# Optimization experiments

Measured on AMD Instinct MI355X. Metric: run time of the kernel, lower is better.

## Reference

```python
import jax, jax.numpy as jnp
import numpy as np

N_NODES = 100000
N_EDGES = 1600000
HIDDEN = 128
BN_EPS = 1e-5


def setup_inputs() -> dict:
    key = jax.random.key(0)
    ks = jax.random.split(key, 6)
    x0 = jax.random.normal(ks[0], (N_NODES, HIDDEN), dtype=jnp.float32)
    x1 = jax.random.normal(ks[1], (N_NODES, HIDDEN), dtype=jnp.float32)
    edge_index = jax.random.randint(ks[2], (2, N_EDGES), 0, N_NODES, dtype=jnp.int64)
    mean_weight = jnp.ones((2,), dtype=jnp.float32)
    # GIN MLP: Linear(h,h) -> ReLU -> Linear(h,h); scale ~ torch default init
    scale = 1.0 / np.sqrt(HIDDEN)
    W1 = jax.random.normal(ks[3], (HIDDEN, HIDDEN), dtype=jnp.float32) * scale
    b1 = jnp.zeros((HIDDEN,), dtype=jnp.float32)
    W2 = jax.random.normal(ks[4], (HIDDEN, HIDDEN), dtype=jnp.float32) * scale
    b2 = jnp.zeros((HIDDEN,), dtype=jnp.float32)
    gamma = jnp.ones((HIDDEN,), dtype=jnp.float32)
    beta = jnp.zeros((HIDDEN,), dtype=jnp.float32)
    return {"x0": x0, "x1": x1, "edge_index": edge_index,
            "mean_weight": mean_weight, "W1": W1, "b1": b1,
            "W2": W2, "b2": b2, "gamma": gamma, "beta": beta}


def reference(x0, x1, edge_index, mean_weight, W1, b1, W2, b2, gamma, beta):
    # sigmoid-gated sum of the two node-feature inputs (no drop-path: deterministic eval)
    s = jax.nn.sigmoid(mean_weight)
    out = s[0] * x0 + s[1] * x1                      # [N, H]
    # GINConv, eps=0: h = MLP(x + sum_{j in N(i)} x_j)
    src, dst = edge_index[0], edge_index[1]
    agg = jax.ops.segment_sum(out[src], dst, num_segments=out.shape[0])  # scatter-add [N, H]
    h = out + agg
    h = jnp.maximum(h @ W1 + b1, 0.0) @ W2 + b2      # Linear-ReLU-Linear
    # BatchNorm1d, training-mode batch statistics (biased variance)
    mean = jnp.mean(h, axis=0)
    var = jnp.var(h, axis=0)
    hn = (h - mean) * jax.lax.rsqrt(var + BN_EPS)
    return hn * gamma + beta
```

## Files before the change

### kernel.cpp

```cpp
#include <hip/hip_runtime.h>
#include <math.h>

#define N_NODES 100000
#define N_EDGES 1600000
#define HID 128
#define BN_EPS 1e-5f
#define BM 64
#define NTILES ((N_NODES + BM - 1) / BM)
#define MLP_BLOCKS 512
#define NSUB 16
#define NPW 4
#define BN_BLOCKS 512

typedef __attribute__((ext_vector_type(8))) short bf16x8;
typedef __attribute__((ext_vector_type(4))) float f32x4;

__device__ inline unsigned short f2bf(float f) {
    unsigned u = __float_as_uint(f);
    unsigned r = u + 0x7FFFu + ((u >> 16) & 1u);
    return (unsigned short)(r >> 16);
}
__device__ inline unsigned pk2(float lo, float hi) {
    return (unsigned)f2bf(lo) | ((unsigned)f2bf(hi) << 16);
}
__device__ inline float bflo(unsigned u) { return __uint_as_float(u << 16); }
__device__ inline float bfhi(unsigned u) { return __uint_as_float(u & 0xffff0000u); }

__global__ __launch_bounds__(256) void k_front(const float* __restrict__ x0,
                                               const float* __restrict__ x1,
                                               const float* __restrict__ mw,
                                               unsigned* __restrict__ gate_u2,
                                               float* __restrict__ shadow,
                                               const float* __restrict__ W1,
                                               const float* __restrict__ W2,
                                               unsigned short* __restrict__ W1T,
                                               unsigned short* __restrict__ W2T,
                                               const int* __restrict__ ei,
                                               int* __restrict__ head,
                                               int2* __restrict__ pair) {
    int bid = blockIdx.x, tid = threadIdx.x;
    int role = bid % 3;
    if (role < 2) {
        int gid = (bid / 3) * 2 + role;
        int t = gid * 256 + tid;
        if (gid < 64) {
            shadow[t] = 0.0f;
            int k = t >> 7, n = t & 127;
            W1T[n * HID + k] = f2bf(W1[t]);
            W2T[n * HID + k] = f2bf(W2[t]);
        }
        float s0 = 1.0f / (1.0f + expf(-mw[0]));
        float s1 = 1.0f / (1.0f + expf(-mw[1]));
        float4 a = ((const float4*)x0)[t];
        float4 b = ((const float4*)x1)[t];
        uint2 o;
        o.x = pk2(s0 * a.x + s1 * b.x, s0 * a.y + s1 * b.y);
        o.y = pk2(s0 * a.z + s1 * b.z, s0 * a.w + s1 * b.w);
        ((uint2*)gate_u2)[t] = o;
    } else {
        int e = (bid / 3) * 256 + tid;
        int src = ei[e];
        int dst = ei[N_EDGES + e];
        int old = atomicExch(&head[(e & (NSUB - 1)) * N_NODES + dst], e);
        pair[e] = make_int2(src, old);
    }
}

__global__ __launch_bounds__(256) void k_agg(const unsigned* __restrict__ gu,
                                             const int2* __restrict__ pair,
                                             const int* __restrict__ head,
                                             unsigned* __restrict__ hbuf_u) {
    int wid = threadIdx.x >> 6, lane = threadIdx.x & 63;
    int nbase = (blockIdx.x * 4 + wid) * NPW;
    int e = head[(lane & 15) * N_NODES + (nbase + (lane >> 4))];

    float sx[NPW], sy[NPW];
#pragma unroll
    for (int j = 0; j < NPW; ++j) {
        unsigned g = gu[(size_t)(nbase + j) * 64 + lane];
        sx[j] = bflo(g); sy[j] = bfhi(g);
    }

    while (__any(e >= 0)) {
        int2 pv = make_int2(-1, -1);
        if (e >= 0) pv = pair[e];
#pragma unroll
        for (int j = 0; j < 64; ++j) {
            int sv = __builtin_amdgcn_readlane(pv.x, j);
            if (sv >= 0) {
                unsigned v = gu[(size_t)sv * 64 + lane];
                sx[j >> 4] += bflo(v);
                sy[j >> 4] += bfhi(v);
            }
        }
        e = pv.y;
    }
#pragma unroll
    for (int j = 0; j < NPW; ++j)
        hbuf_u[(size_t)(nbase + j) * 64 + lane] = pk2(sx[j], sy[j]);
}

__global__ __launch_bounds__(256, 2) void k_mlp(unsigned short* __restrict__ hbuf,
                                                const unsigned short* __restrict__ W1T,
                                                const unsigned short* __restrict__ W2T,
                                                const float* __restrict__ b1,
                                                const float* __restrict__ b2,
                                                float* __restrict__ shadow) {
    __shared__ short lds_x[BM * HID];
    __shared__ short lds_w1[HID * HID];
    __shared__ short lds_w2[HID * HID];

    const int tid = threadIdx.x;

    for (int c = tid; c < 2048; c += 256) {
        int n = c >> 4, k16 = c & 15;
        int4 v1 = ((const int4*)W1T)[c];
        int4 v2 = ((const int4*)W2T)[c];
        int boff = n * 256 + ((k16 * 16) ^ ((n & 7) << 4));
        *(int4*)((char*)lds_w1 + boff) = v1;
        *(int4*)((char*)lds_w2 + boff) = v2;
    }

    const int wid = tid >> 6, lane = tid & 63;
    const int wrow = wid >> 1, wcol = wid & 1;
    const int l15 = lane & 15, l4 = lane >> 4;

    float b1g[4], b2g[4];
#pragma unroll
    for (int nf = 0; nf < 4; ++nf) {
        int n = wcol * 64 + nf * 16 + l15;
        b1g[nf] = b1[n];
        b2g[nf] = b2[n];
    }

    float psum[4] = {0.f, 0.f, 0.f, 0.f}, psq[4] = {0.f, 0.f, 0.f, 0.f};

    __syncthreads();

    for (int tile = blockIdx.x; tile < NTILES; tile += MLP_BLOCKS) {
        const int m0 = tile * BM;

        for (int c = tid; c < BM * 16; c += 256) {
            int r = c >> 4, k16 = c & 15;
            int row = m0 + r;
            int4 v = {0, 0, 0, 0};
            if (row < N_NODES)
                v = ((const int4*)(hbuf + (size_t)row * HID))[k16];
            int boff = r * 256 + ((k16 * 16) ^ ((r & 7) << 4));
            *(int4*)((char*)lds_x + boff) = v;
        }
        __syncthreads();

        f32x4 acc1[2][4];
#pragma unroll
        for (int mf = 0; mf < 2; ++mf)
#pragma unroll
            for (int nf = 0; nf < 4; ++nf) acc1[mf][nf] = (f32x4){0.f, 0.f, 0.f, 0.f};

#pragma unroll
        for (int kc = 0; kc < 4; ++kc) {
            bf16x8 av[2], bv[4];
#pragma unroll
            for (int mf = 0; mf < 2; ++mf) {
                int r = wrow * 32 + mf * 16 + l15;
                int boff = r * 256 + (((kc * 64) + l4 * 16) ^ ((r & 7) << 4));
                av[mf] = *(const bf16x8*)((const char*)lds_x + boff);
            }
#pragma unroll
            for (int nf = 0; nf < 4; ++nf) {
                int n = wcol * 64 + nf * 16 + l15;
                int boff = n * 256 + (((kc * 64) + l4 * 16) ^ ((n & 7) << 4));
                bv[nf] = *(const bf16x8*)((const char*)lds_w1 + boff);
            }
#pragma unroll
            for (int mf = 0; mf < 2; ++mf)
#pragma unroll
                for (int nf = 0; nf < 4; ++nf)
                    acc1[mf][nf] = __builtin_amdgcn_mfma_f32_16x16x32_bf16(av[mf], bv[nf], acc1[mf][nf], 0, 0, 0);
        }

        __syncthreads();

#pragma unroll
        for (int mf = 0; mf < 2; ++mf)
#pragma unroll
            for (int nf = 0; nf < 4; ++nf) {
                int n = wcol * 64 + nf * 16 + l15;
#pragma unroll
                for (int r = 0; r < 4; ++r) {
                    int row = wrow * 32 + mf * 16 + l4 * 4 + r;
                    float v = fmaxf(acc1[mf][nf][r] + b1g[nf], 0.f);
                    int boff = row * 256 + ((2 * n) ^ ((row & 7) << 4));
                    *(unsigned short*)((char*)lds_x + boff) = f2bf(v);
                }
            }

        __syncthreads();

        f32x4 acc2[2][4];
#pragma unroll
        for (int mf = 0; mf < 2; ++mf)
#pragma unroll
            for (int nf = 0; nf < 4; ++nf) acc2[mf][nf] = (f32x4){0.f, 0.f, 0.f, 0.f};

#pragma unroll
        for (int kc = 0; kc < 4; ++kc) {
            bf16x8 av[2], bv[4];
#pragma unroll
            for (int mf = 0; mf < 2; ++mf) {
                int r = wrow * 32 + mf * 16 + l15;
                int boff = r * 256 + (((kc * 64) + l4 * 16) ^ ((r & 7) << 4));
                av[mf] = *(const bf16x8*)((const char*)lds_x + boff);
            }
#pragma unroll
            for (int nf = 0; nf < 4; ++nf) {
                int n = wcol * 64 + nf * 16 + l15;
                int boff = n * 256 + (((kc * 64) + l4 * 16) ^ ((n & 7) << 4));
                bv[nf] = *(const bf16x8*)((const char*)lds_w2 + boff);
            }
#pragma unroll
            for (int mf = 0; mf < 2; ++mf)
#pragma unroll
                for (int nf = 0; nf < 4; ++nf)
                    acc2[mf][nf] = __builtin_amdgcn_mfma_f32_16x16x32_bf16(av[mf], bv[nf], acc2[mf][nf], 0, 0, 0);
        }

#pragma unroll
        for (int mf = 0; mf < 2; ++mf)
#pragma unroll
            for (int nf = 0; nf < 4; ++nf) {
                int n = wcol * 64 + nf * 16 + l15;
#pragma unroll
                for (int r = 0; r < 4; ++r) {
                    int row = m0 + wrow * 32 + mf * 16 + l4 * 4 + r;
                    float v = acc2[mf][nf][r] + b2g[nf];
                    if (row < N_NODES) {
                        unsigned short q = f2bf(v);
                        float vq = __uint_as_float(((unsigned)q) << 16);
                        hbuf[(size_t)row * HID + n] = q;
                        psum[nf] += vq;
                        psq[nf] += vq * vq;
                    }
                }
            }

        __syncthreads();
    }

    float* cs = (float*)lds_x;
    cs[tid] = 0.f;
    __syncthreads();
#pragma unroll
    for (int nf = 0; nf < 4; ++nf) {
        float s = psum[nf], q = psq[nf];
        s += __shfl_xor(s, 16); q += __shfl_xor(q, 16);
        s += __shfl_xor(s, 32); q += __shfl_xor(q, 32);
        if (lane < 16) {
            int n = wcol * 64 + nf * 16 + lane;
            atomicAdd(&cs[n], s);
            atomicAdd(&cs[HID + n], q);
        }
    }
    __syncthreads();
    atomicAdd(&shadow[(blockIdx.x & 63) * 256 + tid], cs[tid]);
}

__global__ __launch_bounds__(256) void k_bn2(const unsigned short* __restrict__ h2,
                                             const float* __restrict__ shadow,
                                             const float* __restrict__ gamma,
                                             const float* __restrict__ beta,
                                             float* __restrict__ out) {
    __shared__ float sc[256];
    int tid = threadIdx.x;
    if (tid < 128) {
        float sum = 0.f, sq = 0.f;
        for (int i = 0; i < 64; ++i) {
            sum += shadow[i * 256 + tid];
            sq  += shadow[i * 256 + 128 + tid];
        }
        float mean = sum * (1.0f / N_NODES);
        float var  = sq * (1.0f / N_NODES) - mean * mean;
        float r = rsqrtf(var + BN_EPS);
        float scale = gamma[tid] * r;
        sc[tid]       = scale;
        sc[128 + tid] = beta[tid] - mean * scale;
    }
    __syncthreads();
    int c4 = tid & 31;
    float4 scale = ((const float4*)sc)[c4];
    float4 shift = ((const float4*)sc)[32 + c4];
    const int total = N_NODES * HID / 4;
    for (int t = blockIdx.x * 256 + tid; t < total; t += BN_BLOCKS * 256) {
        uint2 hv = ((const uint2*)h2)[t];
        float4 o;
        o.x = bflo(hv.x) * scale.x + shift.x;
        o.y = bfhi(hv.x) * scale.y + shift.y;
        o.z = bflo(hv.y) * scale.z + shift.z;
        o.w = bfhi(hv.y) * scale.w + shift.w;
        ((float4*)out)[t] = o;
    }
}

extern "C" void kernel_launch(void* const* d_in, const int* in_sizes, int n_in,
                              void* d_out, int out_size, void* d_ws, size_t ws_size,
                              hipStream_t stream) {
    const float* x0 = (const float*)d_in[0];
    const float* x1 = (const float*)d_in[1];
    const int*   ei = (const int*)d_in[2];
    const float* mw = (const float*)d_in[3];
    const float* W1 = (const float*)d_in[4];
    const float* b1 = (const float*)d_in[5];
    const float* W2 = (const float*)d_in[6];
    const float* b2 = (const float*)d_in[7];
    const float* gamma = (const float*)d_in[8];
    const float* beta  = (const float*)d_in[9];

    float* out = (float*)d_out;

    unsigned short* hbuf = (unsigned short*)d_ws;
    float* shadow = (float*)(hbuf + (size_t)N_NODES * HID);
    float* sc     = shadow + 16384;
    unsigned short* W1T = (unsigned short*)(sc + 256);
    unsigned short* W2T = W1T + 16384;
    int* head    = (int*)(W2T + 16384);
    int2* pair   = (int2*)(head + NSUB * N_NODES);

    hipMemsetAsync(head, 0xFF, (size_t)NSUB * N_NODES * sizeof(int), stream);

    k_front<<<18750, 256, 0, stream>>>(x0, x1, mw, (unsigned*)out, shadow,
                                       W1, W2, W1T, W2T, ei, head, pair);
    k_agg<<<N_NODES / (4 * NPW), 256, 0, stream>>>((const unsigned*)out, pair, head,
                                                   (unsigned*)hbuf);
    k_mlp<<<MLP_BLOCKS, 256, 0, stream>>>(hbuf, W1T, W2T, b1, b2, shadow);
    k_bn2<<<BN_BLOCKS, 256, 0, stream>>>(hbuf, shadow, gamma, beta, out);
}
```

Measured before the change: 242.1 us.

## Prefetch next MLP tile into registers and make head array node-major

The MLP kernel now loads the next tile's aggregated features from global memory into registers during the second GEMM, so the global load latency overlaps compute instead of stalling before each tile. The linked-list head array is switched from sub-list-major to node-major layout, so the 16 sub-list heads of a node are contiguous for the aggregation kernel's initial read and for the atomics. The prefetch costs extra registers, which may reduce occupancy.

```diff
diff --git a/kernel.cpp b/kernel.cpp
--- a/kernel.cpp
+++ b/kernel.cpp
@@ -61,7 +61,7 @@
         int e = (bid / 3) * 256 + tid;
         int src = ei[e];
         int dst = ei[N_EDGES + e];
-        int old = atomicExch(&head[(e & (NSUB - 1)) * N_NODES + dst], e);
+        int old = atomicExch(&head[dst * NSUB + (e & (NSUB - 1))], e);
         pair[e] = make_int2(src, old);
     }
 }
@@ -72,7 +72,7 @@
                                              unsigned* __restrict__ hbuf_u) {
     int wid = threadIdx.x >> 6, lane = threadIdx.x & 63;
     int nbase = (blockIdx.x * 4 + wid) * NPW;
-    int e = head[(lane & 15) * N_NODES + (nbase + (lane >> 4))];
+    int e = head[(nbase + (lane >> 4)) * NSUB + (lane & 15)];
 
     float sx[NPW], sy[NPW];
 #pragma unroll
@@ -135,19 +135,28 @@
 
     float psum[4] = {0.f, 0.f, 0.f, 0.f}, psq[4] = {0.f, 0.f, 0.f, 0.f};
 
+    int4 xr[4];
+    int tile0 = blockIdx.x;
+#pragma unroll
+    for (int i = 0; i < 4; ++i) {
+        int c = tid + i * 256;
+        int row = tile0 * BM + (c >> 4);
+        xr[i] = make_int4(0, 0, 0, 0);
+        if (tile0 < NTILES && row < N_NODES)
+            xr[i] = ((const int4*)(hbuf + (size_t)row * HID))[c & 15];
+    }
+
     __syncthreads();
 
     for (int tile = blockIdx.x; tile < NTILES; tile += MLP_BLOCKS) {
         const int m0 = tile * BM;
 
-        for (int c = tid; c < BM * 16; c += 256) {
+#pragma unroll
+        for (int i = 0; i < 4; ++i) {
+            int c = tid + i * 256;
             int r = c >> 4, k16 = c & 15;
-            int row = m0 + r;
-            int4 v = {0, 0, 0, 0};
-            if (row < N_NODES)
-                v = ((const int4*)(hbuf + (size_t)row * HID))[k16];
             int boff = r * 256 + ((k16 * 16) ^ ((r & 7) << 4));
-            *(int4*)((char*)lds_x + boff) = v;
+            *(int4*)((char*)lds_x + boff) = xr[i];
         }
         __syncthreads();
 
@@ -196,6 +205,17 @@
             }
 
         __syncthreads();
+
+        int tnext = tile + MLP_BLOCKS;
+#pragma unroll
+        for (int i = 0; i < 4; ++i) {
+            int c = tid + i * 256;
+            int row = tnext * BM + (c >> 4);
+            int4 v = make_int4(0, 0, 0, 0);
+            if (tnext < NTILES && row < N_NODES)
+                v = ((const int4*)(hbuf + (size_t)row * HID))[c & 15];
+            xr[i] = v;
+        }
 
         f32x4 acc2[2][4];
 #pragma unroll
```

New measurement: 238.0 us (median of 2 runs). Within noise of the previous version (-1.7%).

## Fuse neighbor aggregation into MLP kernel, writing aggregated tile directly to LDS

Applied to the files above, without the earlier changes.

The separate aggregation kernel is folded into the MLP kernel. Each wave now gathers neighbor sums for 16 nodes (4 linked-list sublists per node instead of 16) and writes the bf16 result straight into the swizzled LDS tile. The head array is re-laid-out node-major. This removes one kernel launch and the global round trip of the aggregated features. In exchange, the MLP kernel runs at 2 blocks/CU with only 512 blocks, so the latency-bound gather gets much less parallelism than the old 6250-block aggregation launch. Each list is also longer with 4 sublists, so lanes idle more in the while loop.

```diff
diff --git a/kernel.cpp b/kernel.cpp
--- a/kernel.cpp
+++ b/kernel.cpp
@@ -7,9 +7,8 @@
 #define BN_EPS 1e-5f
 #define BM 64
 #define NTILES ((N_NODES + BM - 1) / BM)
-#define MLP_BLOCKS 512
-#define NSUB 16
-#define NPW 4
+#define FUSED_BLOCKS 512
+#define NSUB 4
 #define BN_BLOCKS 512
 
 typedef __attribute__((ext_vector_type(8))) short bf16x8;
@@ -61,51 +60,20 @@
         int e = (bid / 3) * 256 + tid;
         int src = ei[e];
         int dst = ei[N_EDGES + e];
-        int old = atomicExch(&head[(e & (NSUB - 1)) * N_NODES + dst], e);
+        int old = atomicExch(&head[dst * NSUB + (e & (NSUB - 1))], e);
         pair[e] = make_int2(src, old);
     }
 }
 
-__global__ __launch_bounds__(256) void k_agg(const unsigned* __restrict__ gu,
-                                             const int2* __restrict__ pair,
-                                             const int* __restrict__ head,
-                                             unsigned* __restrict__ hbuf_u) {
-    int wid = threadIdx.x >> 6, lane = threadIdx.x & 63;
-    int nbase = (blockIdx.x * 4 + wid) * NPW;
-    int e = head[(lane & 15) * N_NODES + (nbase + (lane >> 4))];
-
-    float sx[NPW], sy[NPW];
-#pragma unroll
-    for (int j = 0; j < NPW; ++j) {
-        unsigned g = gu[(size_t)(nbase + j) * 64 + lane];
-        sx[j] = bflo(g); sy[j] = bfhi(g);
-    }
-
-    while (__any(e >= 0)) {
-        int2 pv = make_int2(-1, -1);
-        if (e >= 0) pv = pair[e];
-#pragma unroll
-        for (int j = 0; j < 64; ++j) {
-            int sv = __builtin_amdgcn_readlane(pv.x, j);
-            if (sv >= 0) {
-                unsigned v = gu[(size_t)sv * 64 + lane];
-                sx[j >> 4] += bflo(v);
-                sy[j >> 4] += bfhi(v);
-            }
-        }
-        e = pv.y;
-    }
-#pragma unroll
-    for (int j = 0; j < NPW; ++j)
-        hbuf_u[(size_t)(nbase + j) * 64 + lane] = pk2(sx[j], sy[j]);
-}
-
-__global__ __launch_bounds__(256, 2) void k_mlp(unsigned short* __restrict__ hbuf,
-                                                const unsigned short* __restrict__ W1T,
-                                                const unsigned short* __restrict__ W2T,
-                                                const float* __restrict__ b1,
-                                                const float* __restrict__ b2,
-                                                float* __restrict__ shadow) {
+__global__ __launch_bounds__(256, 2) void k_fused(const unsigned* __restrict__ gu,
+                                                  const int2* __restrict__ pair,
+                                                  const int* __restrict__ head,
+                                                  unsigned short* __restrict__ h2buf,
+                                                  const unsigned short* __restrict__ W1T,
+                                                  const unsigned short* __restrict__ W2T,
+                                                  const float* __restrict__ b1,
+                                                  const float* __restrict__ b2,
+                                                  float* __restrict__ shadow) {
     __shared__ short lds_x[BM * HID];
     __shared__ short lds_w1[HID * HID];
     __shared__ short lds_w2[HID * HID];
@@ -137,17 +105,40 @@
 
     __syncthreads();
 
-    for (int tile = blockIdx.x; tile < NTILES; tile += MLP_BLOCKS) {
+    for (int tile = blockIdx.x; tile < NTILES; tile += FUSED_BLOCKS) {
         const int m0 = tile * BM;
 
-        for (int c = tid; c < BM * 16; c += 256) {
-            int r = c >> 4, k16 = c & 15;
-            int row = m0 + r;
-            int4 v = {0, 0, 0, 0};
-            if (row < N_NODES)
-                v = ((const int4*)(hbuf + (size_t)row * HID))[k16];
-            int boff = r * 256 + ((k16 * 16) ^ ((r & 7) << 4));
-            *(int4*)((char*)lds_x + boff) = v;
+        int mynode = m0 + wid * 16 + (lane >> 2);
+        int e = (mynode < N_NODES) ? head[mynode * NSUB + (lane & 3)] : -1;
+
+        float sx[16], sy[16];
+#pragma unroll
+        for (int j = 0; j < 16; ++j) {
+            int row = m0 + wid * 16 + j;
+            unsigned g = (row < N_NODES) ? gu[(size_t)row * 64 + lane] : 0u;
+            sx[j] = bflo(g); sy[j] = bfhi(g);
+        }
+
+        while (__any(e >= 0)) {
+            int2 pv = make_int2(-1, -1);
+            if (e >= 0) pv = pair[e];
+#pragma unroll
+            for (int j = 0; j < 64; ++j) {
+                int sv = __builtin_amdgcn_readlane(pv.x, j);
+                if (sv >= 0) {
+                    unsigned v = gu[(size_t)sv * 64 + lane];
+                    sx[j >> 2] += bflo(v);
+                    sy[j >> 2] += bfhi(v);
+                }
+            }
+            e = pv.y;
+        }
+
+#pragma unroll
+        for (int j = 0; j < 16; ++j) {
+            int r = wid * 16 + j;
+            int boff = r * 256 + ((lane * 4) ^ ((r & 7) << 4));
+            *(unsigned*)((char*)lds_x + boff) = pk2(sx[j], sy[j]);
         }
         __syncthreads();
 
@@ -237,7 +228,7 @@
                     if (row < N_NODES) {
                         unsigned short q = f2bf(v);
                         float vq = __uint_as_float(((unsigned)q) << 16);
-                        hbuf[(size_t)row * HID + n] = q;
+                        h2buf[(size_t)row * HID + n] = q;
                         psum[nf] += vq;
                         psq[nf] += vq * vq;
                     }
@@ -319,8 +310,7 @@
 
     unsigned short* hbuf = (unsigned short*)d_ws;
     float* shadow = (float*)(hbuf + (size_t)N_NODES * HID);
-    float* sc     = shadow + 16384;
-    unsigned short* W1T = (unsigned short*)(sc + 256);
+    unsigned short* W1T = (unsigned short*)(shadow + 16384);
     unsigned short* W2T = W1T + 16384;
     int* head    = (int*)(W2T + 16384);
     int2* pair   = (int2*)(head + NSUB * N_NODES);
@@ -329,8 +319,7 @@
 
     k_front<<<18750, 256, 0, stream>>>(x0, x1, mw, (unsigned*)out, shadow,
                                        W1, W2, W1T, W2T, ei, head, pair);
-    k_agg<<<N_NODES / (4 * NPW), 256, 0, stream>>>((const unsigned*)out, pair, head,
-                                                   (unsigned*)hbuf);
-    k_mlp<<<MLP_BLOCKS, 256, 0, stream>>>(hbuf, W1T, W2T, b1, b2, shadow);
+    k_fused<<<FUSED_BLOCKS, 256, 0, stream>>>((const unsigned*)out, pair, head, hbuf,
+                                              W1T, W2T, b1, b2, shadow);
     k_bn2<<<BN_BLOCKS, 256, 0, stream>>>(hbuf, shadow, gamma, beta, out);
 }
```

After: 477.6 us. 1.97x slower.
